# Kernel tuning notes

Hardware: AMD Instinct MI355X
Metric: run time of the kernel (lower is better)

Reference implementation:

```python
import jax, jax.numpy as jnp
from jax import lax
import numpy as np

KS, STRIDE, RATE, SCALE = 3, 1, 2, 10.0  # module init kwargs


def _resize_bilinear_ac(x, oh, ow):
    # F.interpolate(mode='bilinear', align_corners=True); x: [B,C,H,W]
    H, W = x.shape[2], x.shape[3]
    ys = jnp.linspace(0.0, H - 1.0, oh)
    xs = jnp.linspace(0.0, W - 1.0, ow)
    y0 = jnp.floor(ys).astype(jnp.int32)
    y1 = jnp.minimum(y0 + 1, H - 1)
    wy = (ys - y0)[:, None]
    x0 = jnp.floor(xs).astype(jnp.int32)
    x1 = jnp.minimum(x0 + 1, W - 1)
    wx = xs - x0
    g = lambda yi, xi: x[:, :, yi, :][:, :, :, xi]
    top = g(y0, x0) * (1 - wx) + g(y0, x1) * wx
    bot = g(y1, x0) * (1 - wx) + g(y1, x1) * wx
    return top * (1 - wy) + bot * wy


def _conv3x3(x, w, b):
    y = lax.conv_general_dilated(x, w, (1, 1), ((1, 1), (1, 1)),
                                 dimension_numbers=('NCHW', 'OIHW', 'NCHW'))
    return y + b[None, :, None, None]


def _extract_patches(x, k, s):
    # mirrors extract_patches(): ZeroPad2d(1) when k != 1, then unfold h,w
    if k != 1:
        x = jnp.pad(x, ((0, 0), (0, 0), (1, 1), (1, 1)))
    b, c, h, w = x.shape
    nh = (h - k) // s + 1
    nw = (w - k) // s + 1
    cols = jnp.stack([x[:, :, i:i + s * (nh - 1) + 1:s, j:j + s * (nw - 1) + 1:s]
                      for i in range(k) for j in range(k)], axis=-1)  # [B,C,nh,nw,k*k]
    return cols.reshape(b, c, nh, nw, k, k).transpose(0, 2, 3, 1, 4, 5).reshape(b, nh * nw, c, k, k)


def _instance_norm(x, eps=1e-5):
    mu = x.mean((2, 3), keepdims=True)
    var = ((x - mu) ** 2).mean((2, 3), keepdims=True)
    return (x - mu) * lax.rsqrt(var + eps)


def _conv_transpose(att, w):
    # torch F.conv_transpose2d(att, w, stride=2, padding=1); att [Q,h,w], w [Q,Cout,4,4]
    rhs = jnp.flip(w, (-2, -1)).transpose(1, 0, 2, 3)  # [Cout,Q,4,4]
    return lax.conv_general_dilated(att[None], rhs, (1, 1), ((2, 2), (2, 2)),
                                    lhs_dilation=(2, 2),
                                    dimension_numbers=('NCHW', 'OIHW', 'NCHW'))[0]


def _forward(background, foreground, mask, Wc, bc, Wm, bm, Wf, bf):
    h, w = foreground.shape[2], foreground.shape[3]
    mask64 = _resize_bilinear_ac(mask, h, w)
    fg_c = foreground * (1 - mask64)
    fg_m = foreground * mask64
    bg_c = background * (1 - mask64)
    bg_m = background * mask64
    # ODConv2d(fg, bg) stand-in: plain 3x3 conv on the fused features
    bg_c = _conv3x3(fg_c + bg_c, Wc, bc)
    bg_m = _conv3x3(fg_m + bg_m, Wm, bm)
    x = _conv3x3(bg_c + bg_m, Wf, bf)
    x = _instance_norm(x)
    x = x * jax.nn.sigmoid(x)  # MemoryEfficientSwish
    b = x.shape[0]
    raw_w = _extract_patches(x, 2 * RATE, STRIDE * RATE)       # [B,1024,256,4,4]
    x_down = _resize_bilinear_ac(x, h // RATE, w // RATE)       # [B,256,32,32]
    hd, wd = x_down.shape[2], x_down.shape[3]
    pt = _extract_patches(x_down, KS, STRIDE)                   # [B,1024,256,3,3]
    mask32 = _resize_bilinear_ac(mask64, hd, wd)
    mpt = _extract_patches(mask32, KS, STRIDE)                  # [B,1024,1,3,3]
    mm = (mpt.mean((2, 3, 4)) == 0.0).astype(x.dtype)[:, :, None, None]  # [B,1024,1,1]
    norm = jnp.sqrt((pt * pt).sum((2, 3, 4), keepdims=True))
    w_normed = pt / jnp.maximum(norm, 1e-4)
    # score = F.conv2d(x_down, w_normed, padding=1): batched patch-attention GEMM
    score = jnp.einsum('bqckl,bpckl->bqp', w_normed, pt).reshape(b, hd * wd, hd, wd)
    score = score * mm
    att = jax.nn.softmax(score * SCALE, axis=1) * mm
    att = jnp.clip(att, 1e-8, None)
    f1 = jax.vmap(_conv_transpose)(att, raw_w) / 4.0            # [B,256,64,64]
    return f1 * mask64 + x * (1 - mask64)


def setup_inputs() -> dict:
    key = jax.random.key(0)
    ks = jax.random.split(key, 9)
    B, C, H, W = 8, 256, 64, 64
    background = jax.random.normal(ks[0], (B, C, H, W), jnp.float32)
    foreground = jax.random.normal(ks[1], (B, C, H, W), jnp.float32)
    # blocky binary hole mask (16x16 blocks upsampled to 256x256)
    m0 = (jax.random.uniform(ks[2], (B, 1, 16, 16)) > 0.5).astype(jnp.float32)
    mask = jnp.repeat(jnp.repeat(m0, 16, axis=2), 16, axis=3)
    s = 0.05
    Wc = jax.random.normal(ks[3], (256, 256, 3, 3), jnp.float32) * s
    bc = jax.random.normal(ks[4], (256,), jnp.float32) * s
    Wm = jax.random.normal(ks[5], (256, 256, 3, 3), jnp.float32) * s
    bm = jax.random.normal(ks[6], (256,), jnp.float32) * s
    Wf = jax.random.normal(ks[7], (256, 256, 3, 3), jnp.float32) * s
    bf = jax.random.normal(ks[8], (256,), jnp.float32) * s
    return {'background': background, 'foreground': foreground, 'mask': mask,
            'Wc': Wc, 'bc': bc, 'Wm': Wm, 'bm': bm, 'Wf': Wf, 'bf': bf}


def reference(background, foreground, mask, Wc, bc, Wm, bm, Wf, bf):
    return _forward(background, foreground, mask, Wc, bc, Wm, bm, Wf, bf)
```

## Files before the change

kernel.cpp:

```cpp
#include <hip/hip_runtime.h>
#include <math.h>

#define B_ 8
#define C_ 256
#define NPIX 4096
#define NP 1024

typedef __attribute__((ext_vector_type(8))) short bf16x8;
typedef __attribute__((ext_vector_type(4))) float f32x4;

#define GLL16(src, dst) __builtin_amdgcn_global_load_lds( \
    (__attribute__((address_space(1))) void*)(src), \
    (__attribute__((address_space(3))) void*)(dst), 16, 0, 0)

__device__ __forceinline__ unsigned short f2bf(float f) {
  unsigned int u = __float_as_uint(f);
  unsigned int r = (u + 0x7FFFu + ((u >> 16) & 1u)) >> 16;
  return (unsigned short)r;
}
__device__ __forceinline__ unsigned int pk2(unsigned short lo, unsigned short hi) {
  return (unsigned int)lo | ((unsigned int)hi << 16);
}

__device__ __forceinline__ float wave_reduce_sum(float v) {
#pragma unroll
  for (int off = 32; off > 0; off >>= 1) v += __shfl_down(v, off, 64);
  return v;
}
__device__ __forceinline__ float wave_reduce_max(float v) {
#pragma unroll
  for (int off = 32; off > 0; off >>= 1) v = fmaxf(v, __shfl_down(v, off, 64));
  return v;
}

__global__ __launch_bounds__(256) void k_resize(const float* __restrict__ in, float* __restrict__ out,
                                                int IH, int IW, int OH, int OW, int nElem) {
  int idx = blockIdx.x * 256 + threadIdx.x;
  if (idx >= nElem) return;
  int ox = idx % OW; int t = idx / OW; int oy = t % OH; int bc = t / OH;
  float dy = (float)(IH - 1) / (float)(OH - 1);
  float dx = (float)(IW - 1) / (float)(OW - 1);
  float yf = (float)oy * dy;
  float xf = (float)ox * dx;
  float y0f = floorf(yf), x0f = floorf(xf);
  int y0 = (int)y0f, x0 = (int)x0f;
  int y1 = min(y0 + 1, IH - 1), x1 = min(x0 + 1, IW - 1);
  float wy = yf - y0f, wx = xf - x0f;
  const float* p = in + (size_t)bc * IH * IW;
  float a = p[y0 * IW + x0], b = p[y0 * IW + x1];
  float c = p[y1 * IW + x0], d = p[y1 * IW + x1];
  float top = a * (1.0f - wx) + b * wx;
  float bot = c * (1.0f - wx) + d * wx;
  out[idx] = top * (1.0f - wy) + bot * wy;
}

__global__ __launch_bounds__(256) void k_wprep(const float* __restrict__ Wc, const float* __restrict__ Wm,
                                               const float* __restrict__ Wf,
                                               unsigned short* __restrict__ Wp1, unsigned short* __restrict__ Wp2) {
  int idx = blockIdx.x * 256 + threadIdx.x;
  if (idx >= 3 * 589824) return;
  int part = idx / 589824;
  int rem = idx % 589824;
  int kk = rem >> 16, co = (rem >> 8) & 255, ci = rem & 255;
  const float* W = (part == 0) ? Wc : (part == 1) ? Wm : Wf;
  unsigned short o = f2bf(W[(size_t)co * 2304 + ci * 9 + kk]);
  if (part == 0) Wp1[rem] = o;
  else if (part == 1) Wp1[589824 + rem] = o;
  else Wp2[rem] = o;
}

__global__ __launch_bounds__(256) void k_bias(const float* __restrict__ bc, const float* __restrict__ bm,
                                              float* __restrict__ bias1, float* __restrict__ zpg) {
  int i = threadIdx.x;
  bias1[i] = bc[i] + bm[i];
  for (int j = i; j < 2048; j += 256) zpg[j] = 0.f;
}

__global__ __launch_bounds__(256) void k_prepAT(const float* __restrict__ fg, const float* __restrict__ bg,
                                                const float* __restrict__ m64,
                                                unsigned short* __restrict__ A0t, unsigned short* __restrict__ A1t) {
  __shared__ unsigned short T0[64][66];
  __shared__ unsigned short T1[64][66];
  int pt = blockIdx.x, ct = blockIdx.y, b = blockIdx.z;
  int pix0 = pt << 6, ci0 = ct << 6;
  int tid = threadIdx.x;
  {
    int r = tid >> 2, c4 = (tid & 3) << 4;
    size_t ib = (((size_t)(b * 256 + ci0 + r)) << 12) + pix0 + c4;
    const float* fb = fg + ib;
    const float* gb = bg + ib;
    const float* mb = m64 + (((size_t)b) << 12) + pix0 + c4;
#pragma unroll
    for (int k = 0; k < 16; k += 4) {
      float4 f = *(const float4*)(fb + k);
      float4 g = *(const float4*)(gb + k);
      float4 m = *(const float4*)(mb + k);
      float s0 = f.x + g.x, s1 = f.y + g.y, s2 = f.z + g.z, s3 = f.w + g.w;
      T0[r][c4 + k + 0] = f2bf(s0 * (1.f - m.x));
      T0[r][c4 + k + 1] = f2bf(s1 * (1.f - m.y));
      T0[r][c4 + k + 2] = f2bf(s2 * (1.f - m.z));
      T0[r][c4 + k + 3] = f2bf(s3 * (1.f - m.w));
      T1[r][c4 + k + 0] = f2bf(s0 * m.x);
      T1[r][c4 + k + 1] = f2bf(s1 * m.y);
      T1[r][c4 + k + 2] = f2bf(s2 * m.z);
      T1[r][c4 + k + 3] = f2bf(s3 * m.w);
    }
  }
  __syncthreads();
  {
    int pr = tid >> 2, cc = (tid & 3) << 4;
    unsigned int o0[8], o1[8];
#pragma unroll
    for (int k = 0; k < 8; k++) {
      o0[k] = pk2(T0[cc + 2 * k][pr], T0[cc + 2 * k + 1][pr]);
      o1[k] = pk2(T1[cc + 2 * k][pr], T1[cc + 2 * k + 1][pr]);
    }
    size_t ob = ((((size_t)b << 12) + pix0 + pr) << 8) + ci0 + cc;
    *(uint4*)&A0t[ob] = *(uint4*)&o0[0];
    *(uint4*)&A0t[ob + 8] = *(uint4*)&o0[4];
    *(uint4*)&A1t[ob] = *(uint4*)&o1[0];
    *(uint4*)&A1t[ob + 8] = *(uint4*)&o1[4];
  }
}

__device__ __forceinline__ int swz(int row, int slot) {
  return row * 32 + ((slot ^ (row & 3) ^ ((row >> 2) & 3)) << 3);
}

template <int NKK, bool OUT_TRANS_BF16>
__global__ __launch_bounds__(256, 2) void k_conv2ph(const unsigned short* __restrict__ A0t,
                                                    const unsigned short* __restrict__ A1t,
                                                    const unsigned short* __restrict__ Wp,
                                                    const float* __restrict__ bias,
                                                    const unsigned short* __restrict__ zp,
                                                    void* __restrict__ outp) {
  __shared__ __align__(16) unsigned short AB[2][16384];
  int wgl = blockIdx.x + 32 * (blockIdx.y + 2 * blockIdx.z);
  int nid = (wgl & 7) * 64 + (wgl >> 3);
  int bp = nid & 31, cot = (nid >> 5) & 1, b = nid >> 6;
  int tid = threadIdx.x, lane = tid & 63, w3 = tid >> 6;
  int wm = w3 >> 1, wn = w3 & 1;

  int rA = w3 * 32 + (lane >> 2), rA1 = rA + 16;
  int ds0 = (lane & 3) ^ (rA & 3) ^ ((rA >> 2) & 3);
  int ds1 = (lane & 3) ^ (rA1 & 3) ^ ((rA1 >> 2) & 3);
  int y_0 = bp * 2 + (rA >> 6), x_0 = rA & 63;
  int y_1 = bp * 2 + (rA1 >> 6), x_1 = rA1 & 63;
  int co_0 = cot * 128 + rA, co_1 = cot * 128 + rA1;

  f32x4 acc[4][4];
#pragma unroll
  for (int i = 0; i < 4; i++)
#pragma unroll
    for (int j = 0; j < 4; j++) acc[i][j] = (f32x4){0.f, 0.f, 0.f, 0.f};

  const unsigned short *pA0, *pA1, *pB0, *pB1;

#define UPDATE(kkv) {                                                           \
    int kk_ = (kkv);                                                            \
    int kw_ = (NKK == 18 && kk_ >= 9) ? kk_ - 9 : kk_;                          \
    const unsigned short* Asrc_ = (NKK == 18 && kk_ >= 9) ? A1t : A0t;          \
    int ky_ = kw_ / 3 - 1, kx_ = kw_ % 3 - 1;                                   \
    int yy0_ = y_0 + ky_, xx0_ = x_0 + kx_;                                     \
    int yy1_ = y_1 + ky_, xx1_ = x_1 + kx_;                                     \
    pA0 = ((unsigned)yy0_ < 64u && (unsigned)xx0_ < 64u)                        \
        ? Asrc_ + ((((size_t)(b << 6) + yy0_) << 6) + xx0_) * 256 + ds0 * 8     \
        : zp + ds0 * 8;                                                         \
    pA1 = ((unsigned)yy1_ < 64u && (unsigned)xx1_ < 64u)                        \
        ? Asrc_ + ((((size_t)(b << 6) + yy1_) << 6) + xx1_) * 256 + ds1 * 8     \
        : zp + ds1 * 8;                                                         \
    pB0 = Wp + ((size_t)kk_ << 16) + co_0 * 256 + ds0 * 8;                      \
    pB1 = Wp + ((size_t)kk_ << 16) + co_1 * 256 + ds1 * 8;                      \
  }
#define STAGE(c2, buf) {                                                        \
    int ci0_ = ((c2) & 3) << 6;                                                 \
    unsigned short* lb_ = &AB[buf][0];                                          \
    GLL16(pA0 + ci0_,      lb_ + w3 * 1024);                                    \
    GLL16(pA1 + ci0_,      lb_ + w3 * 1024 + 512);                              \
    GLL16(pA0 + ci0_ + 32, lb_ + 4096 + w3 * 1024);                             \
    GLL16(pA1 + ci0_ + 32, lb_ + 4096 + w3 * 1024 + 512);                       \
    GLL16(pB0 + ci0_,      lb_ + 8192 + w3 * 1024);                             \
    GLL16(pB1 + ci0_,      lb_ + 8192 + w3 * 1024 + 512);                       \
    GLL16(pB0 + ci0_ + 32, lb_ + 12288 + w3 * 1024);                            \
    GLL16(pB1 + ci0_ + 32, lb_ + 12288 + w3 * 1024 + 512);                      \
  }

  const int NCH = NKK * 4;
  UPDATE(0);
  STAGE(0, 0);
  for (int c = 0; c < NCH; ++c) {
    asm volatile("" ::: "memory");
    __builtin_amdgcn_s_barrier();
    asm volatile("" ::: "memory");
    if (c < NCH - 1) {
      int cn = c + 1;
      if ((cn & 3) == 0) UPDATE(cn >> 2);
      STAGE(cn, cn & 1);
      asm volatile("s_waitcnt vmcnt(8)" ::: "memory");
    } else {
      asm volatile("s_waitcnt vmcnt(0)" ::: "memory");
    }
    __builtin_amdgcn_s_barrier();
    asm volatile("" ::: "memory");
    int slot = lane >> 4;
    int mr = wm * 64 + (lane & 15), ncc = wn * 64 + (lane & 15);
#pragma unroll
    for (int ks = 0; ks < 2; ++ks) {
      const unsigned short* Al = &AB[c & 1][ks << 12];
      const unsigned short* Bl = &AB[c & 1][8192 + (ks << 12)];
      bf16x8 af[4], bfr[4];
#pragma unroll
      for (int i = 0; i < 4; i++) af[i] = *(const bf16x8*)&Al[swz(mr + i * 16, slot)];
#pragma unroll
      for (int j = 0; j < 4; j++) bfr[j] = *(const bf16x8*)&Bl[swz(ncc + j * 16, slot)];
#pragma unroll
      for (int i = 0; i < 4; i++)
#pragma unroll
        for (int j = 0; j < 4; j++)
          acc[i][j] = __builtin_amdgcn_mfma_f32_16x16x32_bf16(af[i], bfr[j], acc[i][j], 0, 0, 0);
    }
  }
#undef STAGE
#undef UPDATE

  int px0 = bp * 128 + wm * 64 + ((lane >> 4) << 2);
  int co0 = cot * 128 + wn * 64 + (lane & 15);
#pragma unroll
  for (int j = 0; j < 4; j++) {
    int co = co0 + j * 16;
    float bs = bias[co];
#pragma unroll
    for (int i = 0; i < 4; i++) {
#pragma unroll
      for (int r = 0; r < 4; r++) {
        float v = acc[i][j][r] + bs;
        int pix = px0 + i * 16 + r;
        if (OUT_TRANS_BF16)
          ((unsigned short*)outp)[((((size_t)b << 12) + pix) << 8) + co] = f2bf(v);
        else
          ((float*)outp)[((((size_t)b << 8) + co) << 12) + pix] = v;
      }
    }
  }
}

__global__ __launch_bounds__(256) void k_post(float* __restrict__ x, float* __restrict__ xd) {
  __shared__ float sL[4096];
  __shared__ float s4[4];
  int bc = blockIdx.x;
  float* p = x + (size_t)bc * NPIX;
  int tid = threadIdx.x;
  int lane = tid & 63, w = tid >> 6;
  float v[16];
  float s = 0.f;
#pragma unroll
  for (int i = 0; i < 16; i++) { v[i] = p[tid + i * 256]; s += v[i]; }
  s = wave_reduce_sum(s);
  if (lane == 0) s4[w] = s;
  __syncthreads();
  float mean = (s4[0] + s4[1] + s4[2] + s4[3]) * (1.0f / 4096.0f);
  __syncthreads();
  float s2 = 0.f;
#pragma unroll
  for (int i = 0; i < 16; i++) { float d = v[i] - mean; s2 += d * d; }
  s2 = wave_reduce_sum(s2);
  if (lane == 0) s4[w] = s2;
  __syncthreads();
  float var = (s4[0] + s4[1] + s4[2] + s4[3]) * (1.0f / 4096.0f);
  float inv = 1.0f / sqrtf(var + 1e-5f);
#pragma unroll
  for (int i = 0; i < 16; i++) {
    float xn = (v[i] - mean) * inv;
    float sg = 1.0f / (1.0f + expf(-xn));
    float o = xn * sg;
    p[tid + i * 256] = o;
    sL[tid + i * 256] = o;
  }
  __syncthreads();
  float dyx = 63.0f / 31.0f;
  float* xdp = xd + (size_t)bc * NP;
#pragma unroll
  for (int k = 0; k < 4; k++) {
    int q = tid + k * 256;
    int yq = q >> 5, xq = q & 31;
    float yf = (float)yq * dyx;
    float xf = (float)xq * dyx;
    float y0f = floorf(yf), x0f = floorf(xf);
    int y0 = (int)y0f, x0 = (int)x0f;
    int y1 = min(y0 + 1, 63), x1 = min(x0 + 1, 63);
    float wy = yf - y0f, wx = xf - x0f;
    float a = sL[y0 * 64 + x0], b2 = sL[y0 * 64 + x1];
    float c2 = sL[y1 * 64 + x0], d2 = sL[y1 * 64 + x1];
    float top = a * (1.0f - wx) + b2 * wx;
    float bot = c2 * (1.0f - wx) + d2 * wx;
    xdp[q] = top * (1.0f - wy) + bot * wy;
  }
}

__global__ __launch_bounds__(256) void k_trans_xd(const float* __restrict__ xd,
                                                  unsigned short* __restrict__ xdt) {
  __shared__ unsigned short T[64][66];
  int qt = blockIdx.x, ct = blockIdx.y, b = blockIdx.z;
  int q0 = qt << 6, ci0 = ct << 6;
  int tid = threadIdx.x;
  {
    int r = tid >> 2, c4 = (tid & 3) << 4;
    const float* xb = xd + (((size_t)(b * 256 + ci0 + r)) << 10) + q0 + c4;
#pragma unroll
// ... 67 lines not shown
  int wgl = blockIdx.x + 8 * (blockIdx.y + 8 * blockIdx.z);
  int nid = (wgl & 7) * 64 + (wgl >> 3);
  int bp = nid & 7, bq = (nid >> 3) & 7, b = nid >> 6;
  int tid = threadIdx.x, lane = tid & 63, w3 = tid >> 6;
  int wm = w3 >> 1, wn = w3 & 1;

  int rA = w3 * 32 + (lane >> 2), rA1 = rA + 16;
  int ds0 = (lane & 3) ^ (rA & 3) ^ ((rA >> 2) & 3);
  int ds1 = (lane & 3) ^ (rA1 & 3) ^ ((rA1 >> 2) & 3);
  int pA0r = bp * 128 + rA, pA1r = bp * 128 + rA1;
  int pB0r = bq * 128 + rA, pB1r = bq * 128 + rA1;
  int piA0 = pA0r >> 5, pjA0 = pA0r & 31, piA1 = pA1r >> 5, pjA1 = pA1r & 31;
  int piB0 = pB0r >> 5, pjB0 = pB0r & 31, piB1 = pB1r >> 5, pjB1 = pB1r & 31;
  const unsigned short* xb = xdt + (((size_t)b) << 18);

  f32x4 acc[4][4];
#pragma unroll
  for (int i = 0; i < 4; i++)
#pragma unroll
    for (int j = 0; j < 4; j++) acc[i][j] = (f32x4){0.f, 0.f, 0.f, 0.f};

  const unsigned short *pA0, *pA1, *pB0, *pB1;

#define GUPDATE(kkv) {                                                          \
    int kk_ = (kkv);                                                            \
    int dy_ = kk_ / 3 - 1, dx_ = kk_ % 3 - 1;                                   \
    int ya0 = piA0 + dy_, xa0 = pjA0 + dx_;                                     \
    int ya1 = piA1 + dy_, xa1 = pjA1 + dx_;                                     \
    int yb0 = piB0 + dy_, xb0 = pjB0 + dx_;                                     \
    int yb1 = piB1 + dy_, xb1 = pjB1 + dx_;                                     \
    pA0 = ((unsigned)ya0 < 32u && (unsigned)xa0 < 32u)                          \
        ? xb + ((((size_t)ya0 << 5) + xa0) << 8) + ds0 * 8 : zp + ds0 * 8;      \
    pA1 = ((unsigned)ya1 < 32u && (unsigned)xa1 < 32u)                          \
        ? xb + ((((size_t)ya1 << 5) + xa1) << 8) + ds1 * 8 : zp + ds1 * 8;      \
    pB0 = ((unsigned)yb0 < 32u && (unsigned)xb0 < 32u)                          \
        ? xb + ((((size_t)yb0 << 5) + xb0) << 8) + ds0 * 8 : zp + ds0 * 8;      \
    pB1 = ((unsigned)yb1 < 32u && (unsigned)xb1 < 32u)                          \
        ? xb + ((((size_t)yb1 << 5) + xb1) << 8) + ds1 * 8 : zp + ds1 * 8;      \
  }
#define GSTAGE(c2, buf) {                                                       \
    int ci0_ = ((c2) & 3) << 6;                                                 \
    unsigned short* lb_ = &AB[buf][0];                                          \
    GLL16(pA0 + ci0_,      lb_ + w3 * 1024);                                    \
    GLL16(pA1 + ci0_,      lb_ + w3 * 1024 + 512);                              \
    GLL16(pA0 + ci0_ + 32, lb_ + 4096 + w3 * 1024);                             \
    GLL16(pA1 + ci0_ + 32, lb_ + 4096 + w3 * 1024 + 512);                       \
    GLL16(pB0 + ci0_,      lb_ + 8192 + w3 * 1024);                             \
    GLL16(pB1 + ci0_,      lb_ + 8192 + w3 * 1024 + 512);                       \
    GLL16(pB0 + ci0_ + 32, lb_ + 12288 + w3 * 1024);                            \
    GLL16(pB1 + ci0_ + 32, lb_ + 12288 + w3 * 1024 + 512);                      \
  }

  GUPDATE(0);
  GSTAGE(0, 0);
  for (int c = 0; c < 36; ++c) {
    asm volatile("" ::: "memory");
    __builtin_amdgcn_s_barrier();
    asm volatile("" ::: "memory");
    if (c < 35) {
      int cn = c + 1;
      if ((cn & 3) == 0) GUPDATE(cn >> 2);
      GSTAGE(cn, cn & 1);
      asm volatile("s_waitcnt vmcnt(8)" ::: "memory");
    } else {
      asm volatile("s_waitcnt vmcnt(0)" ::: "memory");
    }
    __builtin_amdgcn_s_barrier();
    asm volatile("" ::: "memory");
    int slot = lane >> 4;
    int mr = wm * 64 + (lane & 15), ncc = wn * 64 + (lane & 15);
#pragma unroll
    for (int ks = 0; ks < 2; ++ks) {
      const unsigned short* Al = &AB[c & 1][ks << 12];
      const unsigned short* Bl = &AB[c & 1][8192 + (ks << 12)];
      bf16x8 af[4], bfr[4];
#pragma unroll
      for (int i = 0; i < 4; i++) af[i] = *(const bf16x8*)&Al[swz(mr + i * 16, slot)];
#pragma unroll
      for (int j = 0; j < 4; j++) bfr[j] = *(const bf16x8*)&Bl[swz(ncc + j * 16, slot)];
#pragma unroll
      for (int i = 0; i < 4; i++)
#pragma unroll
        for (int j = 0; j < 4; j++)
          acc[i][j] = __builtin_amdgcn_mfma_f32_16x16x32_bf16(af[i], bfr[j], acc[i][j], 0, 0, 0);
    }
  }
#undef GSTAGE
#undef GUPDATE

  int q0 = bq * 128 + wn * 64 + (lane & 15);
  int p0 = bp * 128 + wm * 64 + ((lane >> 4) << 2);
#pragma unroll
  for (int j = 0; j < 4; j++) {
    int q = q0 + j * 16;
    float f = fq[(b << 10) + q];
#pragma unroll
    for (int i = 0; i < 4; i++)
#pragma unroll
      for (int r = 0; r < 4; r++)
        sc[((size_t)(b << 10) + (p0 + i * 16 + r)) * NP + q] = acc[i][j][r] * f;
  }
}

__global__ __launch_bounds__(256) void k_softmax(const float* __restrict__ sc, const float* __restrict__ fq,
                                                 unsigned short* __restrict__ attb) {
  __shared__ float s4[4];
  int row = blockIdx.x;
  int b = row >> 10;
  const float* r = sc + (size_t)row * NP;
  int tid = threadIdx.x;
  int lane = tid & 63, w = tid >> 6;
  float4 sv = *(const float4*)&r[tid * 4];
  float l0 = sv.x * 10.f, l1 = sv.y * 10.f, l2 = sv.z * 10.f, l3 = sv.w * 10.f;
  float mx = fmaxf(fmaxf(l0, l1), fmaxf(l2, l3));
  mx = wave_reduce_max(mx);
  if (lane == 0) s4[w] = mx;
  __syncthreads();
  float M = fmaxf(fmaxf(s4[0], s4[1]), fmaxf(s4[2], s4[3]));
  __syncthreads();
  float e0 = expf(l0 - M), e1 = expf(l1 - M), e2 = expf(l2 - M), e3 = expf(l3 - M);
  float s = e0 + e1 + e2 + e3;
  s = wave_reduce_sum(s);
  if (lane == 0) s4[w] = s;
  __syncthreads();
  float inv = 1.0f / (s4[0] + s4[1] + s4[2] + s4[3]);
  const float* fb = fq + b * NP + tid * 4;
  float m0 = fb[0] > 0.f ? 1.f : 0.f;
  float m1 = fb[1] > 0.f ? 1.f : 0.f;
  float m2 = fb[2] > 0.f ? 1.f : 0.f;
  float m3 = fb[3] > 0.f ? 1.f : 0.f;
  float a0 = fmaxf(e0 * inv * m0, 1e-8f);
  float a1 = fmaxf(e1 * inv * m1, 1e-8f);
  float a2 = fmaxf(e2 * inv * m2, 1e-8f);
  float a3 = fmaxf(e3 * inv * m3, 1e-8f);
  uint2 o;
  o.x = pk2(f2bf(a0), f2bf(a1));
  o.y = pk2(f2bf(a2), f2bf(a3));
  *(uint2*)&attb[(size_t)row * NP + tid * 4] = o;
}

__global__ __launch_bounds__(256) void k_xprep(const float* __restrict__ x,
                                               unsigned short* __restrict__ P0,
                                               unsigned short* __restrict__ P1,
                                               unsigned short* __restrict__ P2) {
  int idx = blockIdx.x * 256 + threadIdx.x;
  int xh8 = idx & 3;
  int yh = (idx >> 2) & 31;
  int co = (idx >> 7) & 255;
  int pc = (idx >> 15) & 3;
  int b  = idx >> 17;
  int cy = pc >> 1, cx = pc & 1;
  const float* row = x + ((size_t)(b * 256 + co) * 64 + (2 * yh + cy)) * 64 + 16 * xh8;
  float4 f0 = *(const float4*)(row);
  float4 f1 = *(const float4*)(row + 4);
  float4 f2 = *(const float4*)(row + 8);
  float4 f3 = *(const float4*)(row + 12);
  unsigned short v0 = f2bf(cx ? f0.y : f0.x), v1 = f2bf(cx ? f0.w : f0.z);
  unsigned short v2 = f2bf(cx ? f1.y : f1.x), v3 = f2bf(cx ? f1.w : f1.z);
  unsigned short v4 = f2bf(cx ? f2.y : f2.x), v5 = f2bf(cx ? f2.w : f2.z);
  unsigned short v6 = f2bf(cx ? f3.y : f3.x), v7 = f2bf(cx ? f3.w : f3.z);
  int prev = __shfl_up((int)v7, 1, 64);
  int next = __shfl_down((int)v0, 1, 64);
  unsigned short pv = (xh8 == 0) ? (unsigned short)0 : (unsigned short)prev;
  unsigned short nx = (xh8 == 3) ? (unsigned short)0 : (unsigned short)next;
  size_t base = ((size_t)((b * 4 + pc) * 256 + co) * 32 + yh) * 32 + 8 * xh8;
  uint4 w0 = {pk2(v0, v1), pk2(v2, v3), pk2(v4, v5), pk2(v6, v7)};
  *(uint4*)&P0[base] = w0;
  uint4 w1 = {pk2(pv, v0), pk2(v1, v2), pk2(v3, v4), pk2(v5, v6)};
  *(uint4*)&P1[base] = w1;
  uint4 w2 = {pk2(v1, v2), pk2(v3, v4), pk2(v5, v6), pk2(v7, nx)};
  *(uint4*)&P2[base] = w2;
}

__global__ __launch_bounds__(256, 2) void k_pv(const unsigned short* __restrict__ attb,
                                               const unsigned short* __restrict__ P0,
                                               const unsigned short* __restrict__ P1,
                                               const unsigned short* __restrict__ P2,
                                               const unsigned short* __restrict__ zp,
                                               const float* __restrict__ xbuf,
                                               const float* __restrict__ m64,
                                               float* __restrict__ out) {
  __shared__ __align__(16) unsigned short AB[2][16384];
  int wg = blockIdx.x + blockIdx.y * 8 + blockIdx.z * 16;
  int nid = (wg & 7) * 64 + (wg >> 3);
  int bn = nid & 7, bm = (nid >> 3) & 1, z = nid >> 4;
  int b = z >> 2, cls = z & 3, cy = cls >> 1, cx = cls & 1;
  int tid = threadIdx.x, lane = tid & 63, w3 = tid >> 6;
  int wm = w3 >> 1, wn = w3 & 1;

  int dy1 = cy ? -1 : 1;
  int pio1 = cy ? 1 : -1;
  int pjo1 = cx ? 1 : -1;
  const unsigned short* Pdx = cx ? P1 : P2;

  int rA0 = w3 * 32 + (lane >> 2);
  int rA1 = rA0 + 16;
  int ds0 = (lane & 3) ^ (rA0 & 3) ^ ((rA0 >> 2) & 3);
  int ds1 = (lane & 3) ^ (rA1 & 3) ^ ((rA1 >> 2) & 3);
  int offA0 = ((z * 256 + bm * 128 + rA0) << 10) + ds0 * 8;
  int offA1 = ((z * 256 + bm * 128 + rA1) << 10) + ds1 * 8;

  const unsigned short* attB = attb + ((size_t)b << 20);
  int o0 = bn * 128 + rA0, o1 = bn * 128 + rA1;
  int oy0 = o0 >> 5, ox0 = o0 & 31, oy1 = o1 >> 5, ox1 = o1 & 31;
#define BPTR(oyv, oxv, dsv, tyv, txv) ({                                        \
    int pi = (oyv) + ((tyv) ? pio1 : 0);                                        \
    int pj = (oxv) + ((txv) ? pjo1 : 0);                                        \
    (pi >= 0 && pi < 32 && pj >= 0 && pj < 32)                                  \
        ? attB + (((pi << 5) + pj) << 10) + (dsv) * 8 : zp; })
  const unsigned short* b0t0 = BPTR(oy0, ox0, ds0, 0, 0);
  const unsigned short* b0t1 = BPTR(oy0, ox0, ds0, 0, 1);
  const unsigned short* b0t2 = BPTR(oy0, ox0, ds0, 1, 0);
  const unsigned short* b0t3 = BPTR(oy0, ox0, ds0, 1, 1);
  const unsigned short* b1t0 = BPTR(oy1, ox1, ds1, 0, 0);
  const unsigned short* b1t1 = BPTR(oy1, ox1, ds1, 0, 1);
  const unsigned short* b1t2 = BPTR(oy1, ox1, ds1, 1, 0);
  const unsigned short* b1t3 = BPTR(oy1, ox1, ds1, 1, 1);
#undef BPTR

  f32x4 acc[4][4];
#pragma unroll
  for (int i = 0; i < 4; i++)
#pragma unroll
    for (int j = 0; j < 4; j++) acc[i][j] = (f32x4){0.f, 0.f, 0.f, 0.f};

  int dA0 = w3 * 1024, dA1 = w3 * 1024 + 512;
  int dB0 = 8192 + w3 * 1024, dB1 = 8192 + w3 * 1024 + 512;

#define PHALF(o2, buf, h) {                                                     \
    int t2 = (o2) >> 5, qi = (o2) & 31;                                         \
    int q32 = qi * 32;                                                          \
    const unsigned short* Ab = (t2 & 1) ? Pdx : P0;                             \
    int dyo = (t2 >> 1) ? dy1 * 32 : 0;                                         \
    bool vA = (t2 < 2) || ((dy1 > 0) ? (qi < 31) : (qi > 0));                   \
    if (!vA) Ab = zp;                                                           \
    int oA0 = vA ? offA0 + dyo + q32 : 0;                                       \
    int oA1 = vA ? offA1 + dyo + q32 : 0;                                       \
    unsigned short* lb = &AB[buf][(h) << 12];                                   \
    GLL16(Ab + oA0, lb + dA0);                                                  \
    GLL16(Ab + oA1, lb + dA1);                                                  \
    const unsigned short* sB0 = (t2 == 0 ? b0t0 : t2 == 1 ? b0t1 : t2 == 2 ? b0t2 : b0t3) + q32; \
    const unsigned short* sB1 = (t2 == 0 ? b1t0 : t2 == 1 ? b1t1 : t2 == 2 ? b1t2 : b1t3) + q32; \
    GLL16(sB0, lb + dB0);                                                       \
    GLL16(sB1, lb + dB1);                                                       \
  }
#define PSTAGE(c2, buf) { PHALF(2 * (c2), buf, 0); PHALF(2 * (c2) + 1, buf, 1); }

  PSTAGE(0, 0);
  for (int c = 0; c < 64; ++c) {
    asm volatile("" ::: "memory");
    __builtin_amdgcn_s_barrier();
    asm volatile("" ::: "memory");
    if (c < 63) {
      PSTAGE(c + 1, (c + 1) & 1);
      asm volatile("s_waitcnt vmcnt(8)" ::: "memory");
    } else {
      asm volatile("s_waitcnt vmcnt(0)" ::: "memory");
    }
    __builtin_amdgcn_s_barrier();
    asm volatile("" ::: "memory");
    int slot = lane >> 4;
    int mr = wm * 64 + (lane & 15), ncc = wn * 64 + (lane & 15);
#pragma unroll
    for (int ks = 0; ks < 2; ++ks) {
      const unsigned short* Al = &AB[c & 1][ks << 12];
      const unsigned short* Bl = &AB[c & 1][8192 + (ks << 12)];
      bf16x8 af[4], bfr[4];
#pragma unroll
      for (int i = 0; i < 4; i++) af[i] = *(const bf16x8*)&Al[swz(mr + i * 16, slot)];
#pragma unroll
      for (int j = 0; j < 4; j++) bfr[j] = *(const bf16x8*)&Bl[swz(ncc + j * 16, slot)];
#pragma unroll
      for (int i = 0; i < 4; i++)
#pragma unroll
        for (int j = 0; j < 4; j++)
          acc[i][j] = __builtin_amdgcn_mfma_f32_16x16x32_bf16(af[i], bfr[j], acc[i][j], 0, 0, 0);
    }
  }
#undef PSTAGE
#undef PHALF

  int co0 = bm * 128 + wm * 64 + ((lane >> 4) << 2);
  int oo0 = bn * 128 + wn * 64 + (lane & 15);
#pragma unroll
  for (int j = 0; j < 4; j++) {
    int o = oo0 + j * 16;
    int oy = ((o >> 5) << 1) + cy, ox = ((o & 31) << 1) + cx;
    int opix = oy * 64 + ox;
    float msk = m64[b * NPIX + opix];
    float s = 0.25f * msk, t1m = 1.0f - msk;
#pragma unroll
    for (int i = 0; i < 4; i++) {
#pragma unroll
      for (int r = 0; r < 4; r++) {
        int co = co0 + i * 16 + r;
        size_t xi = (size_t)(b * C_ + co) * NPIX + opix;
        out[xi] = acc[i][j][r] * s + xbuf[xi] * t1m;
      }
    }
  }
}

extern "C" void kernel_launch(void* const* d_in, const int* in_sizes, int n_in,
                              void* d_out, int out_size, void* d_ws, size_t ws_size,
                              hipStream_t stream) {
  const float* bg   = (const float*)d_in[0];
  const float* fg   = (const float*)d_in[1];
  const float* mask = (const float*)d_in[2];
  const float* Wc   = (const float*)d_in[3];
  const float* bc   = (const float*)d_in[4];
  const float* Wm   = (const float*)d_in[5];
  const float* bm   = (const float*)d_in[6];
  const float* Wf   = (const float*)d_in[7];
  const float* bf   = (const float*)d_in[8];
  float* out = (float*)d_out;
  float* w = (float*)d_ws;

  float* mask64 = w;
  float* sq32   = w + 40960;
  float* fq     = w + 49152;
  float* bias1  = w + 57344;
  float* zpage  = w + 57600;
  unsigned short* A0t = (unsigned short*)(w + 65536);
  unsigned short* A1t = (unsigned short*)(w + 65536 + 4194304);
  float* sc = w + 65536;
  unsigned short* P0u = (unsigned short*)(w + 65536);
  unsigned short* P1u = (unsigned short*)(w + 4259840);
  unsigned short* tbuf_t = (unsigned short*)(w + 8454144);
  float* xd = w + 8454144;
  unsigned short* xdt = (unsigned short*)(w + 10551296);
  unsigned short* attb = (unsigned short*)(w + 8454144);
  float* xbuf = w + 12648448;
  unsigned short* Wp1 = (unsigned short*)(w + 21037056);
  unsigned short* Wp2 = (unsigned short*)(w + 21626880);
  unsigned short* P2u = (unsigned short*)(w + 21037056);

  const unsigned short* zp = (const unsigned short*)zpage;

  hipLaunchKernelGGL(k_resize, dim3(128), dim3(256), 0, stream, mask, mask64, 256, 256, 64, 64, 32768);
  hipLaunchKernelGGL(k_wprep, dim3(6912), dim3(256), 0, stream, Wc, Wm, Wf, Wp1, Wp2);
  hipLaunchKernelGGL(k_bias, dim3(1), dim3(256), 0, stream, bc, bm, bias1, zpage);
  hipLaunchKernelGGL(k_prepAT, dim3(64, 4, 8), dim3(256), 0, stream, fg, bg, mask64, A0t, A1t);
  hipLaunchKernelGGL((k_conv2ph<18, true>), dim3(32, 2, 8), dim3(256), 0, stream,
                     A0t, A1t, Wp1, bias1, zp, (void*)tbuf_t);
  hipLaunchKernelGGL((k_conv2ph<9, false>), dim3(32, 2, 8), dim3(256), 0, stream,
                     tbuf_t, tbuf_t, Wp2, bf, zp, (void*)xbuf);
  hipLaunchKernelGGL(k_post, dim3(B_ * C_), dim3(256), 0, stream, xbuf, xd);
  hipLaunchKernelGGL(k_trans_xd, dim3(16, 4, 8), dim3(256), 0, stream, xd, xdt);
  hipLaunchKernelGGL(k_sq32, dim3(32), dim3(256), 0, stream, xd, sq32);
  hipLaunchKernelGGL(k_fq, dim3(32), dim3(256), 0, stream, sq32, mask64, fq);
  hipLaunchKernelGGL(k_gram2ph, dim3(8, 8, 8), dim3(256), 0, stream, xdt, fq, zp, sc);
  hipLaunchKernelGGL(k_softmax, dim3(B_ * NP), dim3(256), 0, stream, sc, fq, attb);
  hipLaunchKernelGGL(k_xprep, dim3(4096), dim3(256), 0, stream, xbuf, P0u, P1u, P2u);
  hipLaunchKernelGGL(k_pv, dim3(8, 2, 32), dim3(256), 0, stream, attb, P0u, P1u, P2u,
                     zp, xbuf, mask64, out);
}
```

Measured before the change: 338.3 us.

## Use 8-wave 256x128 tiles with interleaved prefetch and MFMA phases in conv and PV

The conv and PV GEMM kernels move from 4-wave 128x128 tiles to 8-wave workgroups that cover a 256-row tile, so each B tile loaded into LDS is shared by twice as many rows. The main loop is split into four barrier-separated phases. Each phase issues part of the next chunk's global-to-LDS loads and then runs a group of MFMAs at raised wave priority, overlapping memory traffic with compute. The cost is more barriers per iteration, a larger LDS footprint (96 KB double-buffered), and register pressure at 512 threads with 2 blocks per CU.

```diff
diff --git a/kernel.cpp b/kernel.cpp
--- a/kernel.cpp
+++ b/kernel.cpp
@@ -12,6 +12,8 @@
 #define GLL16(src, dst) __builtin_amdgcn_global_load_lds( \
     (__attribute__((address_space(1))) void*)(src), \
     (__attribute__((address_space(3))) void*)(dst), 16, 0, 0)
+
+#define MFMA16(a, b, c) __builtin_amdgcn_mfma_f32_16x16x32_bf16((a), (b), (c), 0, 0, 0)
 
 __device__ __forceinline__ unsigned short f2bf(float f) {
   unsigned int u = __float_as_uint(f);
@@ -128,25 +130,27 @@
 }
 
 template <int NKK, bool OUT_TRANS_BF16>
-__global__ __launch_bounds__(256, 2) void k_conv2ph(const unsigned short* __restrict__ A0t,
+__global__ __launch_bounds__(512, 2) void k_conv8ph(const unsigned short* __restrict__ A0t,
                                                     const unsigned short* __restrict__ A1t,
                                                     const unsigned short* __restrict__ Wp,
                                                     const float* __restrict__ bias,
                                                     const unsigned short* __restrict__ zp,
                                                     void* __restrict__ outp) {
-  __shared__ __align__(16) unsigned short AB[2][16384];
-  int wgl = blockIdx.x + 32 * (blockIdx.y + 2 * blockIdx.z);
-  int nid = (wgl & 7) * 64 + (wgl >> 3);
-  int bp = nid & 31, cot = (nid >> 5) & 1, b = nid >> 6;
+  __shared__ __align__(16) unsigned short AB[2][24576];
+  int wgl = blockIdx.x;
+  int nid = (wgl & 7) * 32 + (wgl >> 3);
+  int bp = nid & 15, cot = (nid >> 4) & 1, b = nid >> 5;
   int tid = threadIdx.x, lane = tid & 63, w3 = tid >> 6;
   int wm = w3 >> 1, wn = w3 & 1;
 
   int rA = w3 * 32 + (lane >> 2), rA1 = rA + 16;
+  int rB = w3 * 16 + (lane >> 2);
   int ds0 = (lane & 3) ^ (rA & 3) ^ ((rA >> 2) & 3);
   int ds1 = (lane & 3) ^ (rA1 & 3) ^ ((rA1 >> 2) & 3);
-  int y_0 = bp * 2 + (rA >> 6), x_0 = rA & 63;
-  int y_1 = bp * 2 + (rA1 >> 6), x_1 = rA1 & 63;
-  int co_0 = cot * 128 + rA, co_1 = cot * 128 + rA1;
+  int dsB = (lane & 3) ^ (rB & 3) ^ ((rB >> 2) & 3);
+  int y_0 = bp * 4 + (rA >> 6), x_0 = rA & 63;
+  int y_1 = bp * 4 + (rA1 >> 6), x_1 = rA1 & 63;
+  int coB = cot * 128 + rB;
 
   f32x4 acc[4][4];
 #pragma unroll
@@ -154,9 +158,8 @@
 #pragma unroll
     for (int j = 0; j < 4; j++) acc[i][j] = (f32x4){0.f, 0.f, 0.f, 0.f};
 
-  const unsigned short *pA0, *pA1, *pB0, *pB1;
-
-#define UPDATE(kkv) {                                                           \
+  const unsigned short *pA0, *pA1, *pB;
+#define UPD(kkv) {                                                              \
     int kk_ = (kkv);                                                            \
     int kw_ = (NKK == 18 && kk_ >= 9) ? kk_ - 9 : kk_;                          \
     const unsigned short* Asrc_ = (NKK == 18 && kk_ >= 9) ? A1t : A0t;          \
@@ -169,61 +172,90 @@
     pA1 = ((unsigned)yy1_ < 64u && (unsigned)xx1_ < 64u)                        \
         ? Asrc_ + ((((size_t)(b << 6) + yy1_) << 6) + xx1_) * 256 + ds1 * 8     \
         : zp + ds1 * 8;                                                         \
-    pB0 = Wp + ((size_t)kk_ << 16) + co_0 * 256 + ds0 * 8;                      \
-    pB1 = Wp + ((size_t)kk_ << 16) + co_1 * 256 + ds1 * 8;                      \
-  }
-#define STAGE(c2, buf) {                                                        \
-    int ci0_ = ((c2) & 3) << 6;                                                 \
-    unsigned short* lb_ = &AB[buf][0];                                          \
-    GLL16(pA0 + ci0_,      lb_ + w3 * 1024);                                    \
-    GLL16(pA1 + ci0_,      lb_ + w3 * 1024 + 512);                              \
-    GLL16(pA0 + ci0_ + 32, lb_ + 4096 + w3 * 1024);                             \
-    GLL16(pA1 + ci0_ + 32, lb_ + 4096 + w3 * 1024 + 512);                       \
-    GLL16(pB0 + ci0_,      lb_ + 8192 + w3 * 1024);                             \
-    GLL16(pB1 + ci0_,      lb_ + 8192 + w3 * 1024 + 512);                       \
-    GLL16(pB0 + ci0_ + 32, lb_ + 12288 + w3 * 1024);                            \
-    GLL16(pB1 + ci0_ + 32, lb_ + 12288 + w3 * 1024 + 512);                      \
+    pB = Wp + ((size_t)kk_ << 16) + (size_t)coB * 256 + dsB * 8;                \
   }
 
   const int NCH = NKK * 4;
-  UPDATE(0);
-  STAGE(0, 0);
+  UPD(0);
+  {
+    unsigned short* lb = &AB[0][0];
+    GLL16(pA0, lb + w3 * 1024);
+    GLL16(pA1, lb + w3 * 1024 + 512);
+    GLL16(pA0 + 32, lb + 8192 + w3 * 1024);
+    GLL16(pA1 + 32, lb + 8192 + w3 * 1024 + 512);
+    GLL16(pB, lb + 16384 + w3 * 512);
+    GLL16(pB + 32, lb + 20480 + w3 * 512);
+  }
+  asm volatile("s_waitcnt vmcnt(0)" ::: "memory");
+  __builtin_amdgcn_s_barrier();
+  asm volatile("" ::: "memory");
+
+  int slot = lane >> 4;
+  int mr = wm * 64 + (lane & 15), ncc = wn * 64 + (lane & 15);
+
   for (int c = 0; c < NCH; ++c) {
-    asm volatile("" ::: "memory");
-    __builtin_amdgcn_s_barrier();
-    asm volatile("" ::: "memory");
-    if (c < NCH - 1) {
-      int cn = c + 1;
-      if ((cn & 3) == 0) UPDATE(cn >> 2);
-      STAGE(cn, cn & 1);
-      asm volatile("s_waitcnt vmcnt(8)" ::: "memory");
-    } else {
-      asm volatile("s_waitcnt vmcnt(0)" ::: "memory");
-    }
-    __builtin_amdgcn_s_barrier();
-    asm volatile("" ::: "memory");
-    int slot = lane >> 4;
-    int mr = wm * 64 + (lane & 15), ncc = wn * 64 + (lane & 15);
-#pragma unroll
-    for (int ks = 0; ks < 2; ++ks) {
-      const unsigned short* Al = &AB[c & 1][ks << 12];
-      const unsigned short* Bl = &AB[c & 1][8192 + (ks << 12)];
-      bf16x8 af[4], bfr[4];
-#pragma unroll
-      for (int i = 0; i < 4; i++) af[i] = *(const bf16x8*)&Al[swz(mr + i * 16, slot)];
-#pragma unroll
-      for (int j = 0; j < 4; j++) bfr[j] = *(const bf16x8*)&Bl[swz(ncc + j * 16, slot)];
-#pragma unroll
-      for (int i = 0; i < 4; i++)
-#pragma unroll
-        for (int j = 0; j < 4; j++)
-          acc[i][j] = __builtin_amdgcn_mfma_f32_16x16x32_bf16(af[i], bfr[j], acc[i][j], 0, 0, 0);
-    }
-  }
-#undef STAGE
-#undef UPDATE
-
-  int px0 = bp * 128 + wm * 64 + ((lane >> 4) << 2);
+    const unsigned short* Al0 = &AB[c & 1][0];
+    const unsigned short* Al1 = &AB[c & 1][8192];
+    const unsigned short* Bl0 = &AB[c & 1][16384];
+    const unsigned short* Bl1 = &AB[c & 1][20480];
+    unsigned short* lb = &AB[(c & 1) ^ 1][0];
+    bool last = (c == NCH - 1);
+    int cn = c + 1;
+    if (!last && ((cn & 3) == 0)) UPD(cn >> 2);
+    int cin = (cn & 3) << 6;
+
+    bf16x8 af[4], bf0, bf1;
+#pragma unroll
+    for (int i = 0; i < 4; i++) af[i] = *(const bf16x8*)&Al0[swz(mr + i * 16, slot)];
+    bf0 = *(const bf16x8*)&Bl0[swz(ncc, slot)];
+    bf1 = *(const bf16x8*)&Bl0[swz(ncc + 16, slot)];
+    if (!last) { GLL16(pA0 + cin, lb + w3 * 1024); GLL16(pA1 + cin, lb + w3 * 1024 + 512); }
+    asm volatile("" ::: "memory");
+    __builtin_amdgcn_s_barrier();
+    __builtin_amdgcn_s_setprio(1);
+#pragma unroll
+    for (int i = 0; i < 4; i++) { acc[i][0] = MFMA16(af[i], bf0, acc[i][0]); acc[i][1] = MFMA16(af[i], bf1, acc[i][1]); }
+    __builtin_amdgcn_s_setprio(0);
+    asm volatile("" ::: "memory");
+    __builtin_amdgcn_s_barrier();
+    bf0 = *(const bf16x8*)&Bl0[swz(ncc + 32, slot)];
+    bf1 = *(const bf16x8*)&Bl0[swz(ncc + 48, slot)];
+    if (!last) { GLL16(pA0 + cin + 32, lb + 8192 + w3 * 1024); GLL16(pA1 + cin + 32, lb + 8192 + w3 * 1024 + 512); }
+    asm volatile("" ::: "memory");
+    __builtin_amdgcn_s_barrier();
+    __builtin_amdgcn_s_setprio(1);
+#pragma unroll
+    for (int i = 0; i < 4; i++) { acc[i][2] = MFMA16(af[i], bf0, acc[i][2]); acc[i][3] = MFMA16(af[i], bf1, acc[i][3]); }
+    __builtin_amdgcn_s_setprio(0);
+    asm volatile("" ::: "memory");
+    __builtin_amdgcn_s_barrier();
+#pragma unroll
+    for (int i = 0; i < 4; i++) af[i] = *(const bf16x8*)&Al1[swz(mr + i * 16, slot)];
+    bf0 = *(const bf16x8*)&Bl1[swz(ncc, slot)];
+    bf1 = *(const bf16x8*)&Bl1[swz(ncc + 16, slot)];
+    if (!last) { GLL16(pB + cin, lb + 16384 + w3 * 512); GLL16(pB + cin + 32, lb + 20480 + w3 * 512); }
+    asm volatile("" ::: "memory");
+    __builtin_amdgcn_s_barrier();
+    __builtin_amdgcn_s_setprio(1);
+#pragma unroll
+    for (int i = 0; i < 4; i++) { acc[i][0] = MFMA16(af[i], bf0, acc[i][0]); acc[i][1] = MFMA16(af[i], bf1, acc[i][1]); }
+    __builtin_amdgcn_s_setprio(0);
+    asm volatile("" ::: "memory");
+    __builtin_amdgcn_s_barrier();
+    bf0 = *(const bf16x8*)&Bl1[swz(ncc + 32, slot)];
+    bf1 = *(const bf16x8*)&Bl1[swz(ncc + 48, slot)];
+    asm volatile("s_waitcnt vmcnt(0)" ::: "memory");
+    __builtin_amdgcn_s_barrier();
+    __builtin_amdgcn_s_setprio(1);
+#pragma unroll
+    for (int i = 0; i < 4; i++) { acc[i][2] = MFMA16(af[i], bf0, acc[i][2]); acc[i][3] = MFMA16(af[i], bf1, acc[i][3]); }
+    __builtin_amdgcn_s_setprio(0);
+    asm volatile("" ::: "memory");
+    __builtin_amdgcn_s_barrier();
+  }
+#undef UPD
+
+  int px0 = bp * 256 + wm * 64 + ((lane >> 4) << 2);
   int co0 = cot * 128 + wn * 64 + (lane & 15);
 #pragma unroll
   for (int j = 0; j < 4; j++) {
@@ -457,7 +489,7 @@
       for (int i = 0; i < 4; i++)
 #pragma unroll
         for (int j = 0; j < 4; j++)
-          acc[i][j] = __builtin_amdgcn_mfma_f32_16x16x32_bf16(af[i], bfr[j], acc[i][j], 0, 0, 0);
+          acc[i][j] = MFMA16(af[i], bfr[j], acc[i][j]);
     }
   }
 #undef GSTAGE
@@ -547,50 +579,45 @@
   *(uint4*)&P2[base] = w2;
 }
 
-__global__ __launch_bounds__(256, 2) void k_pv(const unsigned short* __restrict__ attb,
-                                               const unsigned short* __restrict__ P0,
-                                               const unsigned short* __restrict__ P1,
-                                               const unsigned short* __restrict__ P2,
-                                               const unsigned short* __restrict__ zp,
-                                               const float* __restrict__ xbuf,
-                                               const float* __restrict__ m64,
-                                               float* __restrict__ out) {
-  __shared__ __align__(16) unsigned short AB[2][16384];
-  int wg = blockIdx.x + blockIdx.y * 8 + blockIdx.z * 16;
-  int nid = (wg & 7) * 64 + (wg >> 3);
-  int bn = nid & 7, bm = (nid >> 3) & 1, z = nid >> 4;
+__global__ __launch_bounds__(512, 2) void k_pv8(const unsigned short* __restrict__ attb,
+                                                const unsigned short* __restrict__ P0_,
+                                                const unsigned short* __restrict__ P1,
+                                                const unsigned short* __restrict__ P2,
+                                                const unsigned short* __restrict__ zp,
+                                                const float* __restrict__ xbuf,
+                                                const float* __restrict__ m64,
+                                                float* __restrict__ out) {
+  __shared__ __align__(16) unsigned short AB[2][24576];
+  int wgl = blockIdx.x;
+  int nid = (wgl & 7) * 32 + (wgl >> 3);
+  int bn = nid & 7, z = nid >> 3;
   int b = z >> 2, cls = z & 3, cy = cls >> 1, cx = cls & 1;
   int tid = threadIdx.x, lane = tid & 63, w3 = tid >> 6;
   int wm = w3 >> 1, wn = w3 & 1;
 
   int dy1 = cy ? -1 : 1;
-  int pio1 = cy ? 1 : -1;
-  int pjo1 = cx ? 1 : -1;
+  int pio1 = cy ? 1 : -1, pjo1 = cx ? 1 : -1;
   const unsigned short* Pdx = cx ? P1 : P2;
 
-  int rA0 = w3 * 32 + (lane >> 2);
-  int rA1 = rA0 + 16;
-  int ds0 = (lane & 3) ^ (rA0 & 3) ^ ((rA0 >> 2) & 3);
+  int rA = w3 * 32 + (lane >> 2), rA1 = rA + 16;
+  int rB = w3 * 16 + (lane >> 2);
+  int ds0 = (lane & 3) ^ (rA & 3) ^ ((rA >> 2) & 3);
   int ds1 = (lane & 3) ^ (rA1 & 3) ^ ((rA1 >> 2) & 3);
-  int offA0 = ((z * 256 + bm * 128 + rA0) << 10) + ds0 * 8;
-  int offA1 = ((z * 256 + bm * 128 + rA1) << 10) + ds1 * 8;
+  int dsB = (lane & 3) ^ (rB & 3) ^ ((rB >> 2) & 3);
+  size_t offA0 = (((size_t)z * 256 + rA) << 10) + ds0 * 8;
+  size_t offA1 = (((size_t)z * 256 + rA1) << 10) + ds1 * 8;
 
   const unsigned short* attB = attb + ((size_t)b << 20);
-  int o0 = bn * 128 + rA0, o1 = bn * 128 + rA1;
-  int oy0 = o0 >> 5, ox0 = o0 & 31, oy1 = o1 >> 5, ox1 = o1 & 31;
-#define BPTR(oyv, oxv, dsv, tyv, txv) ({                                        \
-    int pi = (oyv) + ((tyv) ? pio1 : 0);                                        \
-    int pj = (oxv) + ((txv) ? pjo1 : 0);                                        \
+  int oB = bn * 128 + rB, oyB = oB >> 5, oxB = oB & 31;
+#define BPTR(tyv, txv) ({                                                       \
+    int pi = oyB + ((tyv) ? pio1 : 0);                                          \
+    int pj = oxB + ((txv) ? pjo1 : 0);                                          \
     (pi >= 0 && pi < 32 && pj >= 0 && pj < 32)                                  \
-        ? attB + (((pi << 5) + pj) << 10) + (dsv) * 8 : zp; })
-  const unsigned short* b0t0 = BPTR(oy0, ox0, ds0, 0, 0);
-  const unsigned short* b0t1 = BPTR(oy0, ox0, ds0, 0, 1);
-  const unsigned short* b0t2 = BPTR(oy0, ox0, ds0, 1, 0);
-  const unsigned short* b0t3 = BPTR(oy0, ox0, ds0, 1, 1);
-  const unsigned short* b1t0 = BPTR(oy1, ox1, ds1, 0, 0);
-  const unsigned short* b1t1 = BPTR(oy1, ox1, ds1, 0, 1);
-  const unsigned short* b1t2 = BPTR(oy1, ox1, ds1, 1, 0);
-  const unsigned short* b1t3 = BPTR(oy1, ox1, ds1, 1, 1);
+        ? attB + (((pi << 5) + pj) << 10) + dsB * 8 : zp + dsB * 8; })
+  const unsigned short* bt0 = BPTR(0, 0);
+  const unsigned short* bt1 = BPTR(0, 1);
+  const unsigned short* bt2 = BPTR(1, 0);
+  const unsigned short* bt3 = BPTR(1, 1);
 #undef BPTR
 
   f32x4 acc[4][4];
@@ -599,63 +626,109 @@
 #pragma unroll
     for (int j = 0; j < 4; j++) acc[i][j] = (f32x4){0.f, 0.f, 0.f, 0.f};
 
-  int dA0 = w3 * 1024, dA1 = w3 * 1024 + 512;
-  int dB0 = 8192 + w3 * 1024, dB1 = 8192 + w3 * 1024 + 512;
-
-#define PHALF(o2, buf, h) {                                                     \
-    int t2 = (o2) >> 5, qi = (o2) & 31;                                         \
-    int q32 = qi * 32;                                                          \
-    const unsigned short* Ab = (t2 & 1) ? Pdx : P0;                             \
-    int dyo = (t2 >> 1) ? dy1 * 32 : 0;                                         \
-    bool vA = (t2 < 2) || ((dy1 > 0) ? (qi < 31) : (qi > 0));                   \
-    if (!vA) Ab = zp;                                                           \
-    int oA0 = vA ? offA0 + dyo + q32 : 0;                                       \
-    int oA1 = vA ? offA1 + dyo + q32 : 0;                                       \
-    unsigned short* lb = &AB[buf][(h) << 12];                                   \
-    GLL16(Ab + oA0, lb + dA0);                                                  \
-    GLL16(Ab + oA1, lb + dA1);                                                  \
-    const unsigned short* sB0 = (t2 == 0 ? b0t0 : t2 == 1 ? b0t1 : t2 == 2 ? b0t2 : b0t3) + q32; \
-    const unsigned short* sB1 = (t2 == 0 ? b1t0 : t2 == 1 ? b1t1 : t2 == 2 ? b1t2 : b1t3) + q32; \
-    GLL16(sB0, lb + dB0);                                                       \
-    GLL16(sB1, lb + dB1);                                                       \
-  }
-#define PSTAGE(c2, buf) { PHALF(2 * (c2), buf, 0); PHALF(2 * (c2) + 1, buf, 1); }
-
-  PSTAGE(0, 0);
+#define PV_SRC(cnv)                                                             \
+    int t2n = (cnv) >> 4, qi0n = ((cnv) & 15) << 1;                             \
+    int dyon = (t2n >> 1) ? dy1 * 32 : 0;                                       \
+    const unsigned short* An = (t2n & 1) ? Pdx : P0_;                           \
+    bool vA0 = (t2n < 2) || ((dy1 > 0) ? (qi0n < 31) : (qi0n > 0));             \
+    bool vA1 = (t2n < 2) || ((dy1 > 0) ? (qi0n + 1 < 31) : true);               \
+    const unsigned short* sb = (t2n == 0 ? bt0 : t2n == 1 ? bt1 : t2n == 2 ? bt2 : bt3);
+
+  {
+    PV_SRC(0);
+    unsigned short* lb = &AB[0][0];
+    const unsigned short* sa0 = vA0 ? An + offA0 + dyon + qi0n * 32 : zp + ds0 * 8;
+    const unsigned short* sa1 = vA0 ? An + offA1 + dyon + qi0n * 32 : zp + ds1 * 8;
+    GLL16(sa0, lb + w3 * 1024);
+    GLL16(sa1, lb + w3 * 1024 + 512);
+    const unsigned short* sa2 = vA1 ? An + offA0 + dyon + (qi0n + 1) * 32 : zp + ds0 * 8;
+    const unsigned short* sa3 = vA1 ? An + offA1 + dyon + (qi0n + 1) * 32 : zp + ds1 * 8;
+    GLL16(sa2, lb + 8192 + w3 * 1024);
+    GLL16(sa3, lb + 8192 + w3 * 1024 + 512);
+    GLL16(sb + qi0n * 32, lb + 16384 + w3 * 512);
+    GLL16(sb + (qi0n + 1) * 32, lb + 20480 + w3 * 512);
+  }
+  asm volatile("s_waitcnt vmcnt(0)" ::: "memory");
+  __builtin_amdgcn_s_barrier();
+  asm volatile("" ::: "memory");
+
+  int slot = lane >> 4;
+  int mr = wm * 64 + (lane & 15), ncc = wn * 64 + (lane & 15);
+
   for (int c = 0; c < 64; ++c) {
-    asm volatile("" ::: "memory");
-    __builtin_amdgcn_s_barrier();
-    asm volatile("" ::: "memory");
-    if (c < 63) {
-      PSTAGE(c + 1, (c + 1) & 1);
-      asm volatile("s_waitcnt vmcnt(8)" ::: "memory");
-    } else {
-      asm volatile("s_waitcnt vmcnt(0)" ::: "memory");
-    }
-    __builtin_amdgcn_s_barrier();
-    asm volatile("" ::: "memory");
-    int slot = lane >> 4;
-    int mr = wm * 64 + (lane & 15), ncc = wn * 64 + (lane & 15);
-#pragma unroll
-    for (int ks = 0; ks < 2; ++ks) {
-      const unsigned short* Al = &AB[c & 1][ks << 12];
-      const unsigned short* Bl = &AB[c & 1][8192 + (ks << 12)];
-      bf16x8 af[4], bfr[4];
-#pragma unroll
-      for (int i = 0; i < 4; i++) af[i] = *(const bf16x8*)&Al[swz(mr + i * 16, slot)];
-#pragma unroll
-      for (int j = 0; j < 4; j++) bfr[j] = *(const bf16x8*)&Bl[swz(ncc + j * 16, slot)];
-#pragma unroll
-      for (int i = 0; i < 4; i++)
-#pragma unroll
-        for (int j = 0; j < 4; j++)
-          acc[i][j] = __builtin_amdgcn_mfma_f32_16x16x32_bf16(af[i], bfr[j], acc[i][j], 0, 0, 0);
-    }
-  }
-#undef PSTAGE
-#undef PHALF
-
-  int co0 = bm * 128 + wm * 64 + ((lane >> 4) << 2);
+    const unsigned short* Al0 = &AB[c & 1][0];
+    const unsigned short* Al1 = &AB[c & 1][8192];
+    const unsigned short* Bl0 = &AB[c & 1][16384];
+    const unsigned short* Bl1 = &AB[c & 1][20480];
+    unsigned short* lb = &AB[(c & 1) ^ 1][0];
+    bool last = (c == 63);
+    PV_SRC(c + 1);
+
+    bf16x8 af[4], bf0, bf1;
+#pragma unroll
+    for (int i = 0; i < 4; i++) af[i] = *(const bf16x8*)&Al0[swz(mr + i * 16, slot)];
+    bf0 = *(const bf16x8*)&Bl0[swz(ncc, slot)];
+    bf1 = *(const bf16x8*)&Bl0[swz(ncc + 16, slot)];
+    if (!last) {
+      const unsigned short* sa0 = vA0 ? An + offA0 + dyon + qi0n * 32 : zp + ds0 * 8;
+      const unsigned short* sa1 = vA0 ? An + offA1 + dyon + qi0n * 32 : zp + ds1 * 8;
+      GLL16(sa0, lb + w3 * 1024);
+      GLL16(sa1, lb + w3 * 1024 + 512);
+    }
+    asm volatile("" ::: "memory");
+    __builtin_amdgcn_s_barrier();
+    __builtin_amdgcn_s_setprio(1);
+#pragma unroll
+    for (int i = 0; i < 4; i++) { acc[i][0] = MFMA16(af[i], bf0, acc[i][0]); acc[i][1] = MFMA16(af[i], bf1, acc[i][1]); }
+    __builtin_amdgcn_s_setprio(0);
+    asm volatile("" ::: "memory");
+    __builtin_amdgcn_s_barrier();
+    bf0 = *(const bf16x8*)&Bl0[swz(ncc + 32, slot)];
+    bf1 = *(const bf16x8*)&Bl0[swz(ncc + 48, slot)];
+    if (!last) {
+      const unsigned short* sa2 = vA1 ? An + offA0 + dyon + (qi0n + 1) * 32 : zp + ds0 * 8;
+      const unsigned short* sa3 = vA1 ? An + offA1 + dyon + (qi0n + 1) * 32 : zp + ds1 * 8;
+      GLL16(sa2, lb + 8192 + w3 * 1024);
+      GLL16(sa3, lb + 8192 + w3 * 1024 + 512);
+    }
+    asm volatile("" ::: "memory");
+    __builtin_amdgcn_s_barrier();
+    __builtin_amdgcn_s_setprio(1);
+#pragma unroll
+    for (int i = 0; i < 4; i++) { acc[i][2] = MFMA16(af[i], bf0, acc[i][2]); acc[i][3] = MFMA16(af[i], bf1, acc[i][3]); }
+    __builtin_amdgcn_s_setprio(0);
+    asm volatile("" ::: "memory");
+    __builtin_amdgcn_s_barrier();
+#pragma unroll
+    for (int i = 0; i < 4; i++) af[i] = *(const bf16x8*)&Al1[swz(mr + i * 16, slot)];
+    bf0 = *(const bf16x8*)&Bl1[swz(ncc, slot)];
+    bf1 = *(const bf16x8*)&Bl1[swz(ncc + 16, slot)];
+    if (!last) {
+      GLL16(sb + qi0n * 32, lb + 16384 + w3 * 512);
+      GLL16(sb + (qi0n + 1) * 32, lb + 20480 + w3 * 512);
+    }
+    asm volatile("" ::: "memory");
+    __builtin_amdgcn_s_barrier();
+    __builtin_amdgcn_s_setprio(1);
+#pragma unroll
+    for (int i = 0; i < 4; i++) { acc[i][0] = MFMA16(af[i], bf0, acc[i][0]); acc[i][1] = MFMA16(af[i], bf1, acc[i][1]); }
+    __builtin_amdgcn_s_setprio(0);
+    asm volatile("" ::: "memory");
+    __builtin_amdgcn_s_barrier();
+    bf0 = *(const bf16x8*)&Bl1[swz(ncc + 32, slot)];
+    bf1 = *(const bf16x8*)&Bl1[swz(ncc + 48, slot)];
+    asm volatile("s_waitcnt vmcnt(0)" ::: "memory");
+    __builtin_amdgcn_s_barrier();
+    __builtin_amdgcn_s_setprio(1);
+#pragma unroll
+    for (int i = 0; i < 4; i++) { acc[i][2] = MFMA16(af[i], bf0, acc[i][2]); acc[i][3] = MFMA16(af[i], bf1, acc[i][3]); }
+    __builtin_amdgcn_s_setprio(0);
+    asm volatile("" ::: "memory");
+    __builtin_amdgcn_s_barrier();
+  }
+#undef PV_SRC
+
+  int co0 = wm * 64 + ((lane >> 4) << 2);
   int oo0 = bn * 128 + wn * 64 + (lane & 15);
 #pragma unroll
   for (int j = 0; j < 4; j++) {
@@ -716,9 +789,9 @@
   hipLaunchKernelGGL(k_wprep, dim3(6912), dim3(256), 0, stream, Wc, Wm, Wf, Wp1, Wp2);
   hipLaunchKernelGGL(k_bias, dim3(1), dim3(256), 0, stream, bc, bm, bias1, zpage);
   hipLaunchKernelGGL(k_prepAT, dim3(64, 4, 8), dim3(256), 0, stream, fg, bg, mask64, A0t, A1t);
-  hipLaunchKernelGGL((k_conv2ph<18, true>), dim3(32, 2, 8), dim3(256), 0, stream,
+  hipLaunchKernelGGL((k_conv8ph<18, true>), dim3(256), dim3(512), 0, stream,
                      A0t, A1t, Wp1, bias1, zp, (void*)tbuf_t);
-  hipLaunchKernelGGL((k_conv2ph<9, false>), dim3(32, 2, 8), dim3(256), 0, stream,
+  hipLaunchKernelGGL((k_conv8ph<9, false>), dim3(256), dim3(512), 0, stream,
                      tbuf_t, tbuf_t, Wp2, bf, zp, (void*)xbuf);
   hipLaunchKernelGGL(k_post, dim3(B_ * C_), dim3(256), 0, stream, xbuf, xd);
   hipLaunchKernelGGL(k_trans_xd, dim3(16, 4, 8), dim3(256), 0, stream, xd, xdt);
@@ -727,6 +800,6 @@
   hipLaunchKernelGGL(k_gram2ph, dim3(8, 8, 8), dim3(256), 0, stream, xdt, fq, zp, sc);
   hipLaunchKernelGGL(k_softmax, dim3(B_ * NP), dim3(256), 0, stream, sc, fq, attb);
   hipLaunchKernelGGL(k_xprep, dim3(4096), dim3(256), 0, stream, xbuf, P0u, P1u, P2u);
-  hipLaunchKernelGGL(k_pv, dim3(8, 2, 32), dim3(256), 0, stream, attb, P0u, P1u, P2u,
+  hipLaunchKernelGGL(k_pv8, dim3(256), dim3(512), 0, stream, attb, P0u, P1u, P2u,
                      zp, xbuf, mask64, out);
 }
```

New measurement: 363.7 us. +7.5%, slower.
